# Optimization experiments

Hardware: AMD Instinct MI355X
Metric: run time of the kernel (lower is better)

## Reference

```python
import jax, jax.numpy as jnp
import numpy as np
from jax import lax

B, C, H, W = 8192, 256, 5, 5
G = 8
SE_HID = 64        # max(8, 256 // 4)
GN_EPS = 1e-5
MM_EPS = 1e-8


def group_norm(x, gamma, beta):
    # x: [B, C, H, W]; normalize per (group, H, W)
    b = x.shape[0]
    xg = x.reshape(b, G, C // G, H, W)
    mean = xg.mean(axis=(2, 3, 4), keepdims=True)
    var = xg.var(axis=(2, 3, 4), keepdims=True)
    xg = (xg - mean) * lax.rsqrt(var + GN_EPS)
    xn = xg.reshape(b, C, H, W)
    return xn * gamma[None, :, None, None] + beta[None, :, None, None]


def setup_inputs() -> dict:
    key = jax.random.key(0)
    ks = jax.random.split(key, 10)
    x = jax.random.normal(ks[0], (B, C, H, W), dtype=jnp.float32)
    pair_mask = (jax.random.uniform(ks[1], (B, 1, H, W)) < 0.8).astype(jnp.float32)
    s1 = 1.0 / np.sqrt(C)
    W1 = jax.random.normal(ks[2], (C, C), dtype=jnp.float32) * s1          # 1x1 conv
    W2 = jax.random.normal(ks[3], (C, C, 3, 3), dtype=jnp.float32) * (s1 / 3.0)
    g1 = jnp.ones((C,), jnp.float32); b1 = jnp.zeros((C,), jnp.float32)
    g2 = jnp.ones((C,), jnp.float32); b2 = jnp.zeros((C,), jnp.float32)
    fc1_w = jax.random.normal(ks[4], (SE_HID, C), dtype=jnp.float32) * s1
    fc1_b = jnp.zeros((SE_HID,), jnp.float32)
    fc2_w = jax.random.normal(ks[5], (C, SE_HID), dtype=jnp.float32) / np.sqrt(SE_HID)
    fc2_b = jnp.zeros((C,), jnp.float32)
    return {"x": x, "pair_mask": pair_mask, "W1": W1, "g1": g1, "b1": b1,
            "W2": W2, "g2": g2, "b2": b2,
            "fc1_w": fc1_w, "fc1_b": fc1_b, "fc2_w": fc2_w, "fc2_b": fc2_b}


def reference(x, pair_mask, W1, g1, b1, W2, g2, b2, fc1_w, fc1_b, fc2_w, fc2_b):
    residual = x
    # conv1: 1x1, no bias -> channel mixing
    out = jnp.einsum('bchw,oc->bohw', x, W1)
    out = jax.nn.gelu(group_norm(out, g1, b1), approximate=False)
    # conv2: 3x3, padding=1, no bias
    out = lax.conv_general_dilated(out, W2, window_strides=(1, 1),
                                   padding=((1, 1), (1, 1)),
                                   dimension_numbers=('NCHW', 'OIHW', 'NCHW'))
    out = jax.nn.gelu(group_norm(out, g2, b2), approximate=False)
    out = out + residual
    # masked SE
    denom = jnp.maximum(pair_mask.sum(axis=(-1, -2)), MM_EPS)   # [B,1]
    pooled = (out * pair_mask).sum(axis=(-1, -2)) / denom       # [B,C]
    h = jax.nn.gelu(pooled @ fc1_w.T + fc1_b, approximate=False)
    gate = jax.nn.sigmoid(h @ fc2_w.T + fc2_b)                  # [B,C]
    out = out * gate[:, :, None, None] * pair_mask              # SE mask
    out = out * pair_mask                                       # final mask
    return out, gate
```

## Files before the change

### kernel.cpp

```cpp
#include <hip/hip_runtime.h>
#include <math.h>


typedef short v8s  __attribute__((ext_vector_type(8)));
typedef short v4s  __attribute__((ext_vector_type(4)));
typedef float v16f __attribute__((ext_vector_type(16)));
typedef float v4f  __attribute__((ext_vector_type(4)));

#define NTHREADS 512
#define NB 2
#define CPB 560
#define YROWS 49
#define YSB (YROWS*CPB)

#define Y_BYTES  (NB*YSB)
#define GB_OFF   (Y_BYTES)
#define MASK_OFF (GB_OFF + 4096)
#define POOL_OFF (MASK_OFF + 256)
#define H_OFF    (POOL_OFF + 2048)
#define GATE_OFF (H_OFF + 512)
#define INVD_OFF (GATE_OFF + 2048)
#define SMEM_BYTES (INVD_OFF + 64)

__device__ __forceinline__ unsigned short f2bf(float f){
  unsigned u = __float_as_uint(f);
  u = u + 0x7fffu + ((u >> 16) & 1u);
  return (unsigned short)(u >> 16);
}
__device__ __forceinline__ float gelu_f(float v){
  float z  = fabsf(v) * 0.70710678118654752f;
  float t  = __builtin_amdgcn_rcpf(fmaf(0.3275911f, z, 1.0f));
  float e  = __builtin_amdgcn_exp2f(-z*z*1.4426950408889634f);
  float p  = fmaf(1.061405429f, t, -1.453152027f);
  p = fmaf(p, t, 1.421413741f);
  p = fmaf(p, t, -0.284496736f);
  p = fmaf(p, t, 0.254829592f);
  float er = fmaf(-p*t, e, 1.0f);
  er = __builtin_copysignf(er, v);
  return 0.5f*v*(1.0f + er);
}

__device__ __forceinline__ void v16store(char* dst, const v16f &v){
  #pragma unroll
  for (int q=0;q<4;++q){
    v4f t; t[0]=v[4*q]; t[1]=v[4*q+1]; t[2]=v[4*q+2]; t[3]=v[4*q+3];
    *(v4f*)(dst + q*1024) = t;
  }
}
__device__ __forceinline__ void v16addload(const char* src, v16f &v){
  #pragma unroll
  for (int q=0;q<4;++q){
    v4f t = *(const v4f*)(src + q*1024);
    v[4*q]+=t[0]; v[4*q+1]+=t[1]; v[4*q+2]+=t[2]; v[4*q+3]+=t[3];
  }
}

__global__ void prep_kernel(const float* __restrict__ W1, const float* __restrict__ W2,
                            const float* __restrict__ fc1w, const float* __restrict__ fc2w,
                            unsigned short* __restrict__ w1p, unsigned short* __restrict__ w2p,
                            float* __restrict__ fc1t, float* __restrict__ fc2t)
{
  int t = blockIdx.x*blockDim.x + threadIdx.x;
  int stride = gridDim.x*blockDim.x;
  for (int i=t; i<16*256*16; i+=stride){
    int s=i>>12, o=(i>>4)&255, kk=i&15;
    w1p[i] = f2bf(W1[o*256 + s*16 + kk]);
  }
  for (int i=t; i<144*256*16; i+=stride){
    int s=i>>12, o=(i>>4)&255, kk=i&15;
    int tap=s>>4, cb=s&15;
    w2p[i] = f2bf(W2[o*2304 + (cb*16+kk)*9 + tap]);
  }
  for (int i=t; i<256*64; i+=stride){ int c=i>>6, h=i&63; fc1t[i]=fc1w[h*256+c]; }
  for (int i=t; i<64*256; i+=stride){ int k=i>>8, c=i&255; fc2t[i]=fc2w[c*64+k]; }
}

__global__ __launch_bounds__(NTHREADS, 4) void lrb_main(
    const float* __restrict__ xg, const float* __restrict__ maskg,
    const float* __restrict__ g1, const float* __restrict__ b1,
    const float* __restrict__ g2, const float* __restrict__ b2,
    const unsigned short* __restrict__ w1p, const unsigned short* __restrict__ w2p,
    const float* __restrict__ fc1t, const float* __restrict__ fc1b,
    const float* __restrict__ fc2t, const float* __restrict__ fc2b,
    float* __restrict__ outg, float* __restrict__ gateg)
{
  extern __shared__ char smem[];
  float* OUTF = (float*)smem;
  float* GB   = (float*)(smem + GB_OFF);
  float* MS   = (float*)(smem + MASK_OFF);
  float* POOL = (float*)(smem + POOL_OFF);
  float* HS   = (float*)(smem + H_OFF);
  float* GT   = (float*)(smem + GATE_OFF);
  float* INVD = (float*)(smem + INVD_OFF);

  const int tid  = threadIdx.x;
  const int lane = tid & 63;
  const int wid  = tid >> 6;
  const int mp   = wid >> 1;
  const int kh   = wid & 1;
  const int p    = lane & 31;
  const int half = lane >> 5;
  const int hx   = half << 4;
  const bool pv  = (p < 25);
  const int b0   = blockIdx.x * NB;

  {
    int4 z4; z4.x=z4.y=z4.z=z4.w=0;
    for (int i = tid; i < NB*24*35; i += NTHREADS){
      int nbb = i / 840;
      int rem = i - nbb*840;
      int rr  = 25 + rem/35, cc = rem - (rem/35)*35;
      *(int4*)(smem + nbb*YSB + rr*CPB + cc*16) = z4;
    }
    if (tid < 256){
      GB[tid]=g1[tid]; GB[256+tid]=b1[tid]; GB[512+tid]=g2[tid]; GB[768+tid]=b2[tid];
    }
    if (tid >= 256 && tid < 256 + NB*32){
      int t2 = tid - 256;
      int nbb = t2>>5, pp = t2&31;
      MS[t2] = (pp < 25) ? maskg[(size_t)(b0+nbb)*25 + pp] : 0.f;
    }
  }

  const int pr = p/5, ps = p - 5*(p/5);
  const int pbase = pv ? (7*pr + ps) : 0;
  const int pbCPB = pbase*CPB;
  const int zCPB  = (p-24)*CPB;
  const int bcol  = hx + kh*256;
  const char* w1c = (const char*)w1p;
  const char* w2c = (const char*)w2p;
  const int aoff1 = (wid*32 + p)*32 + hx;
  const char* w2base = w2c + kh*65536 + mp*2048 + p*32 + hx;
  const char* Yb1[2] = { smem + p*CPB + hx, smem + YSB + p*CPB + hx };

  v8s A1[3], B1[3][2];
  #pragma unroll
  for (int s0=0; s0<3; ++s0) A1[s0] = *(const v8s*)(w1c + s0*8192 + aoff1);

  for (int i = tid; i < NB*25*32; i += NTHREADS){
    int nbb = i / 800;
    int rem = i - nbb*800;
    int pp  = rem >> 5;
    int c8  = rem & 31;
    const float* src = xg + ((size_t)(b0+nbb)*256 + c8*8)*25 + pp;
    v8s pk;
    #pragma unroll
    for (int k=0;k<8;++k) pk[k] = (short)f2bf(src[k*25]);
    *(v8s*)(smem + nbb*YSB + pp*CPB + c8*16) = pk;
  }
  __syncthreads();

  if (tid < NB){
    float s=0.f;
    #pragma unroll
    for (int pp=0;pp<25;++pp) s += MS[tid*32+pp];
    INVD[tid] = __builtin_amdgcn_rcpf(fmaxf(s, 1e-8f));
  }

  v16f acc1_0, acc1_1;
  #pragma unroll
  for (int j=0;j<16;++j){ acc1_0[j]=0.f; acc1_1[j]=0.f; }
  #pragma unroll
  for (int s0=0; s0<3; ++s0){
    B1[s0][0] = *(const v8s*)(Yb1[0] + s0*32);
    B1[s0][1] = *(const v8s*)(Yb1[1] + s0*32);
  }
  #pragma unroll
  for (int s=0; s<16; ++s){
    acc1_0 = __builtin_amdgcn_mfma_f32_32x32x16_bf16(A1[s%3], B1[s%3][0], acc1_0, 0,0,0);
    acc1_1 = __builtin_amdgcn_mfma_f32_32x32x16_bf16(A1[s%3], B1[s%3][1], acc1_1, 0,0,0);
    if (s+3 < 16){
      A1[s%3] = *(const v8s*)(w1c + (s+3)*8192 + aoff1);
      B1[s%3][0] = *(const v8s*)(Yb1[0] + (s+3)*32);
      B1[s%3][1] = *(const v8s*)(Yb1[1] + (s+3)*32);
    }
  }

  {
    float s0a=0.f,q0a=0.f,s1a=0.f,q1a=0.f;
    #pragma unroll
    for (int j=0;j<16;++j){
      float v0 = acc1_0[j], v1 = acc1_1[j];
      s0a+=v0; q0a+=v0*v0; s1a+=v1; q1a+=v1*v1;
    }
    #pragma unroll
    for (int off=1; off<64; off<<=1){
      s0a += __shfl_xor(s0a, off, 64); q0a += __shfl_xor(q0a, off, 64);
      s1a += __shfl_xor(s1a, off, 64); q1a += __shfl_xor(q1a, off, 64);
    }
    __syncthreads();

    const int grow = pbase + 8;
    float mu0 = s0a*(1.f/800.f), mu1 = s1a*(1.f/800.f);
    float rstd0 = rsqrtf(q0a*(1.f/800.f) - mu0*mu0 + 1e-5f);
    float rstd1 = rsqrtf(q1a*(1.f/800.f) - mu1*mu1 + 1e-5f);
    if (pv){
      #pragma unroll
      for (int nt=0; nt<2; ++nt){
        float mu = nt ? mu1 : mu0, rstd = nt ? rstd1 : rstd0;
        char* dst = smem + nt*YSB + grow*CPB + wid*64 + half*8;
        #pragma unroll
        for (int q=0;q<4;++q){
          v4s pk;
          #pragma unroll
          for (int i2=0;i2<4;++i2){
            int ch = wid*32 + q*8 + half*4 + i2;
            float v = nt ? acc1_1[4*q+i2] : acc1_0[4*q+i2];
            float f = (v-mu)*rstd*GB[ch]+GB[256+ch];
            pk[i2] = (short)f2bf(gelu_f(f));
          }
          *(v4s*)(dst + q*16) = pk;
        }
      }
    }
  }
  {
    int4 z4; z4.x=z4.y=z4.z=z4.w=0;
    for (int i = tid; i < NB*12*35; i += NTHREADS){
      int nbb = i / 420;
      int rem = i - nbb*420;
      int rr  = rem/35, cc = rem - (rem/35)*35;
      int row = rr < 8 ? rr : (rr < 10 ? rr + 5 : rr + 10);
      *(int4*)(smem + nbb*YSB + row*CPB + cc*16) = z4;
    }
  }

  v8s A2[3][2], B2[3][2];
  #pragma unroll
  for (int s0=0; s0<3; ++s0){
    A2[s0][0] = *(const v8s*)(w2base + (s0>>3)*131072 + (s0&7)*8192);
    A2[s0][1] = *(const v8s*)(w2base + (s0>>3)*131072 + (s0&7)*8192 + 1024);
  }
  __syncthreads();

  v16f acc2_00, acc2_01, acc2_10, acc2_11;
  #pragma unroll
  for (int j=0;j<16;++j){ acc2_00[j]=0.f; acc2_01[j]=0.f; acc2_10[j]=0.f; acc2_11[j]=0.f; }

  {
    constexpr int OFF7[9] = {0,1,2,7,8,9,14,15,16};
    #pragma unroll
    for (int s0=0; s0<3; ++s0){
      int ro = pv ? (pbCPB + OFF7[0]*CPB) : zCPB;
      B2[s0][0] = *(const v8s*)(smem + ro + bcol + (s0&7)*32);
      B2[s0][1] = *(const v8s*)(smem + YSB + ro + bcol + (s0&7)*32);
    }
    #pragma unroll
    for (int s=0; s<72; ++s){
      acc2_00 = __builtin_amdgcn_mfma_f32_32x32x16_bf16(A2[s%3][0], B2[s%3][0], acc2_00, 0,0,0);
      acc2_01 = __builtin_amdgcn_mfma_f32_32x32x16_bf16(A2[s%3][0], B2[s%3][1], acc2_01, 0,0,0);
      acc2_10 = __builtin_amdgcn_mfma_f32_32x32x16_bf16(A2[s%3][1], B2[s%3][0], acc2_10, 0,0,0);
      acc2_11 = __builtin_amdgcn_mfma_f32_32x32x16_bf16(A2[s%3][1], B2[s%3][1], acc2_11, 0,0,0);
      if (s+3 < 72){
        int s3 = s+3;
        A2[s%3][0] = *(const v8s*)(w2base + (s3>>3)*131072 + (s3&7)*8192);
        A2[s%3][1] = *(const v8s*)(w2base + (s3>>3)*131072 + (s3&7)*8192 + 1024);
        int ro = pv ? (pbCPB + OFF7[s3>>3]*CPB) : zCPB;
        B2[s%3][0] = *(const v8s*)(smem + ro + bcol + (s3&7)*32);
        B2[s%3][1] = *(const v8s*)(smem + YSB + ro + bcol + (s3&7)*32);
      }
    }
  }
  __syncthreads();

  {
    char* EXw = smem + (kh^1)*16384 + mp*4096 + (lane<<4);
    const char* EXr = smem + kh*16384 + mp*4096 + (lane<<4);
    if (kh==0) v16store(EXw, acc2_01); else v16store(EXw, acc2_00);
    __syncthreads();
    if (kh==0) v16addload(EXr, acc2_00); else v16addload(EXr, acc2_01);
    __syncthreads();
    if (kh==0) v16store(EXw, acc2_11); else v16store(EXw, acc2_10);
    __syncthreads();
    if (kh==0) v16addload(EXr, acc2_10); else v16addload(EXr, acc2_11);
  }
  v16f F0 = (kh==0) ? acc2_00 : acc2_01;
  v16f F1 = (kh==0) ? acc2_10 : acc2_11;

  {
    float s0a=0.f,q0a=0.f,s1a=0.f,q1a=0.f;
    #pragma unroll
    for (int j=0;j<16;++j){
      float v0=F0[j], v1=F1[j];
      s0a+=v0; q0a+=v0*v0; s1a+=v1; q1a+=v1*v1;
    }
    #pragma unroll
    for (int off=1; off<64; off<<=1){
      s0a += __shfl_xor(s0a, off, 64); q0a += __shfl_xor(q0a, off, 64);
      s1a += __shfl_xor(s1a, off, 64); q1a += __shfl_xor(q1a, off, 64);
    }
    __syncthreads();

    float mu0 = s0a*(1.f/800.f), mu1 = s1a*(1.f/800.f);
    float rstd0 = rsqrtf(q0a*(1.f/800.f) - mu0*mu0 + 1e-5f);
    float rstd1 = rsqrtf(q1a*(1.f/800.f) - mu1*mu1 + 1e-5f);
    float mk = pv ? MS[kh*32+p] : 0.f;
    const float* xr = xg + ((size_t)(b0+kh)*256 + mp*64)*25 + p;
    float ps0[16], ps1[16];
    #pragma unroll
    for (int j=0;j<16;++j){
      int crow = (j&3) + 8*(j>>2) + 4*half;
      {
        int ch = mp*64 + crow;
        float f = (F0[j]-mu0)*rstd0*GB[512+ch]+GB[768+ch];
        f = gelu_f(f);
        if (pv){ f += xr[crow*25]; OUTF[kh*6400 + ch*25 + p] = f; }
        ps0[j] = f*mk;
      }
      {
        int ch = mp*64 + 32 + crow;
        float f = (F1[j]-mu1)*rstd1*GB[512+ch]+GB[768+ch];
        f = gelu_f(f);
        if (pv){ f += xr[(32+crow)*25]; OUTF[kh*6400 + ch*25 + p] = f; }
        ps1[j] = f*mk;
      }
    }
    #pragma unroll
    for (int off=1; off<32; off<<=1)
      #pragma unroll
      for (int j=0;j<16;++j){
        ps0[j] += __shfl_xor(ps0[j], off, 64);
        ps1[j] += __shfl_xor(ps1[j], off, 64);
      }
    if ((lane&31)==0){
      #pragma unroll
      for (int j=0;j<16;++j){
        int crow = (j&3) + 8*(j>>2) + 4*half;
        POOL[kh*256 + mp*64 + crow]      = ps0[j];
        POOL[kh*256 + mp*64 + 32 + crow] = ps1[j];
      }
    }
  }
  __syncthreads();

  {
    int nbb  = tid >> 8;
    int hid  = (tid >> 2) & 63;
    int part = tid & 3;
    const float* pl = POOL + nbb*256 + part*64;
    const float* wp = fc1t + part*64*64 + hid;
    float dot = 0.f;
    #pragma unroll 8
    for (int c=0;c<64;++c) dot += wp[c*64]*pl[c];
    dot += __shfl_xor(dot, 1, 64);
    dot += __shfl_xor(dot, 2, 64);
    if (part == 0)
      HS[nbb*64+hid] = gelu_f(fmaf(INVD[nbb], dot, fc1b[hid]));
  }
  __syncthreads();
  {
    int ch = tid & 255, nbb = tid >> 8;
    const float* hp = HS + nbb*64;
    float dot = 0.f;
    #pragma unroll 8
    for (int k=0;k<64;++k) dot += fc2t[k*256+ch]*hp[k];
    dot += fc2b[ch];
    float gv = __builtin_amdgcn_rcpf(1.0f + __builtin_amdgcn_exp2f(-dot*1.4426950408889634f));
    GT[nbb*256+ch] = gv;
    gateg[(size_t)(b0+nbb)*256+ch] = gv;
  }
  __syncthreads();

  for (int i = tid; i < NB*1600; i += NTHREADS){
    int nbb = i / 1600;
    int r4  = i - nbb*1600;
    int e0  = r4*4;
    v4f o4 = *(const v4f*)(OUTF + nbb*6400 + e0);
    #pragma unroll
    for (int k=0;k<4;++k){
      int e = e0+k;
      int ch = e/25;
      int pp = e - ch*25;
      o4[k] = o4[k] * GT[nbb*256+ch] * MS[nbb*32+pp];
    }
    *(v4f*)(outg + (size_t)(b0+nbb)*6400 + e0) = o4;
  }
}

extern "C" void kernel_launch(void* const* d_in, const int* in_sizes, int n_in,
                              void* d_out, int out_size, void* d_ws, size_t ws_size,
                              hipStream_t stream)
{
  const float* xg   = (const float*)d_in[0];
  const float* pm   = (const float*)d_in[1];
  const float* W1   = (const float*)d_in[2];
  const float* g1   = (const float*)d_in[3];
  const float* b1   = (const float*)d_in[4];
  const float* W2   = (const float*)d_in[5];
  const float* g2   = (const float*)d_in[6];
  const float* b2   = (const float*)d_in[7];
  const float* fc1w = (const float*)d_in[8];
  const float* fc1b = (const float*)d_in[9];
  const float* fc2w = (const float*)d_in[10];
  const float* fc2b = (const float*)d_in[11];

  float* outg  = (float*)d_out;
  float* gateg = outg + (size_t)8192*256*25;

  unsigned short* w1p = (unsigned short*)d_ws;
  unsigned short* w2p = w1p + 16*256*16;
  float* fc1t = (float*)(w2p + 144*256*16);
  float* fc2t = fc1t + 256*64;

  prep_kernel<<<dim3(512), dim3(256), 0, stream>>>(W1, W2, fc1w, fc2w, w1p, w2p, fc1t, fc2t);

  hipFuncSetAttribute(reinterpret_cast<const void*>(lrb_main),
                      hipFuncAttributeMaxDynamicSharedMemorySize, (int)SMEM_BYTES);
  lrb_main<<<dim3(4096), dim3(NTHREADS), SMEM_BYTES, stream>>>(
      xg, pm, g1, b1, g2, b2, w1p, w2p, fc1t, fc1b, fc2t, fc2b, outg, gateg);
}
```

Measured before the change: 615.7 us.

## Restructure conv2 loop per row-tap, add MFMA priority, pool via LDS dot

Repacks W2 so each K-half's taps are laid out contiguously and rewrites the 72-step conv2 MFMA loop as three row passes of 24 steps. Each pass uses a base-offset increment instead of per-step OFF7 table lookups. Adds s_setprio around MFMA groups in both GEMMs so matrix instructions get issue priority over loads. Replaces the shuffle-based masked pooling (16x2 values over 5 xor rounds) with a per-thread 25-element dot over LDS after an extra barrier. The change trades shuffle work and address arithmetic for one more sync and a rolled outer loop.

```diff
diff --git a/kernel.cpp b/kernel.cpp
--- a/kernel.cpp
+++ b/kernel.cpp
@@ -68,8 +68,11 @@
   }
   for (int i=t; i<144*256*16; i+=stride){
     int s=i>>12, o=(i>>4)&255, kk=i&15;
-    int tap=s>>4, cb=s&15;
-    w2p[i] = f2bf(W2[o*2304 + (cb*16+kk)*9 + tap]);
+    int kh = (s >= 72) ? 1 : 0;
+    int r  = s - kh*72;
+    int tap = r>>3, u = r&7;
+    int ck = kh*128 + u*16 + kk;
+    w2p[i] = f2bf(W2[o*2304 + ck*9 + tap]);
   }
   for (int i=t; i<256*64; i+=stride){ int c=i>>6, h=i&63; fc1t[i]=fc1w[h*256+c]; }
   for (int i=t; i<64*256; i+=stride){ int k=i>>8, c=i&255; fc2t[i]=fc2w[c*64+k]; }
@@ -124,13 +127,11 @@
 
   const int pr = p/5, ps = p - 5*(p/5);
   const int pbase = pv ? (7*pr + ps) : 0;
-  const int pbCPB = pbase*CPB;
-  const int zCPB  = (p-24)*CPB;
   const int bcol  = hx + kh*256;
   const char* w1c = (const char*)w1p;
   const char* w2c = (const char*)w2p;
   const int aoff1 = (wid*32 + p)*32 + hx;
-  const char* w2base = w2c + kh*65536 + mp*2048 + p*32 + hx;
+  const char* w2k = w2c + kh*589824 + mp*2048 + p*32 + hx;
   const char* Yb1[2] = { smem + p*CPB + hx, smem + YSB + p*CPB + hx };
 
   v8s A1[3], B1[3][2];
@@ -167,8 +168,10 @@
   }
   #pragma unroll
   for (int s=0; s<16; ++s){
+    __builtin_amdgcn_s_setprio(1);
     acc1_0 = __builtin_amdgcn_mfma_f32_32x32x16_bf16(A1[s%3], B1[s%3][0], acc1_0, 0,0,0);
     acc1_1 = __builtin_amdgcn_mfma_f32_32x32x16_bf16(A1[s%3], B1[s%3][1], acc1_1, 0,0,0);
+    __builtin_amdgcn_s_setprio(0);
     if (s+3 < 16){
       A1[s%3] = *(const v8s*)(w1c + (s+3)*8192 + aoff1);
       B1[s%3][0] = *(const v8s*)(Yb1[0] + (s+3)*32);
@@ -228,8 +231,8 @@
   v8s A2[3][2], B2[3][2];
   #pragma unroll
   for (int s0=0; s0<3; ++s0){
-    A2[s0][0] = *(const v8s*)(w2base + (s0>>3)*131072 + (s0&7)*8192);
-    A2[s0][1] = *(const v8s*)(w2base + (s0>>3)*131072 + (s0&7)*8192 + 1024);
+    A2[s0][0] = *(const v8s*)(w2k + s0*8192);
+    A2[s0][1] = *(const v8s*)(w2k + s0*8192 + 1024);
   }
   __syncthreads();
 
@@ -238,28 +241,46 @@
   for (int j=0;j<16;++j){ acc2_00[j]=0.f; acc2_01[j]=0.f; acc2_10[j]=0.f; acc2_11[j]=0.f; }
 
   {
-    constexpr int OFF7[9] = {0,1,2,7,8,9,14,15,16};
+    int bq = pv ? pbase*CPB : 41*CPB;
+    const int bd = pv ? 7*CPB : 0;
+    int tb = 0;
+
     #pragma unroll
     for (int s0=0; s0<3; ++s0){
-      int ro = pv ? (pbCPB + OFF7[0]*CPB) : zCPB;
-      B2[s0][0] = *(const v8s*)(smem + ro + bcol + (s0&7)*32);
-      B2[s0][1] = *(const v8s*)(smem + YSB + ro + bcol + (s0&7)*32);
-    }
-    #pragma unroll
-    for (int s=0; s<72; ++s){
-      acc2_00 = __builtin_amdgcn_mfma_f32_32x32x16_bf16(A2[s%3][0], B2[s%3][0], acc2_00, 0,0,0);
-      acc2_01 = __builtin_amdgcn_mfma_f32_32x32x16_bf16(A2[s%3][0], B2[s%3][1], acc2_01, 0,0,0);
-      acc2_10 = __builtin_amdgcn_mfma_f32_32x32x16_bf16(A2[s%3][1], B2[s%3][0], acc2_10, 0,0,0);
-      acc2_11 = __builtin_amdgcn_mfma_f32_32x32x16_bf16(A2[s%3][1], B2[s%3][1], acc2_11, 0,0,0);
-      if (s+3 < 72){
-        int s3 = s+3;
-        A2[s%3][0] = *(const v8s*)(w2base + (s3>>3)*131072 + (s3&7)*8192);
-        A2[s%3][1] = *(const v8s*)(w2base + (s3>>3)*131072 + (s3&7)*8192 + 1024);
-        int ro = pv ? (pbCPB + OFF7[s3>>3]*CPB) : zCPB;
-        B2[s%3][0] = *(const v8s*)(smem + ro + bcol + (s3&7)*32);
-        B2[s%3][1] = *(const v8s*)(smem + YSB + ro + bcol + (s3&7)*32);
-      }
-    }
+      B2[s0][0] = *(const v8s*)(smem + bq + bcol + s0*32);
+      B2[s0][1] = *(const v8s*)(smem + YSB + bq + bcol + s0*32);
+    }
+
+#define C2_STEP(S, PF) do { \
+    __builtin_amdgcn_s_setprio(1); \
+    acc2_00 = __builtin_amdgcn_mfma_f32_32x32x16_bf16(A2[(S)%3][0], B2[(S)%3][0], acc2_00, 0,0,0); \
+    acc2_01 = __builtin_amdgcn_mfma_f32_32x32x16_bf16(A2[(S)%3][0], B2[(S)%3][1], acc2_01, 0,0,0); \
+    acc2_10 = __builtin_amdgcn_mfma_f32_32x32x16_bf16(A2[(S)%3][1], B2[(S)%3][0], acc2_10, 0,0,0); \
+    acc2_11 = __builtin_amdgcn_mfma_f32_32x32x16_bf16(A2[(S)%3][1], B2[(S)%3][1], acc2_11, 0,0,0); \
+    __builtin_amdgcn_s_setprio(0); \
+    if (PF) { \
+      const char* ap_ = w2k + tb + ((S)+3)*8192; \
+      A2[(S)%3][0] = *(const v8s*)(ap_); \
+      A2[(S)%3][1] = *(const v8s*)(ap_ + 1024); \
+      const int ro_ = (((S)+3) < 24) ? (((S)+3)>>3)*CPB : 7*CPB; \
+      const int co_ = (((S)+3)&7)*32; \
+      B2[(S)%3][0] = *(const v8s*)(smem + bq + ro_ + bcol + co_); \
+      B2[(S)%3][1] = *(const v8s*)(smem + YSB + bq + ro_ + bcol + co_); \
+    } \
+  } while(0)
+
+    #pragma unroll 1
+    for (int tr=0; tr<2; ++tr){
+      #pragma unroll
+      for (int s=0; s<24; ++s) C2_STEP(s, 1);
+      tb += 196608;
+      bq += bd;
+    }
+    #pragma unroll
+    for (int s=0; s<21; ++s) C2_STEP(s, 1);
+    #pragma unroll
+    for (int s=21; s<24; ++s) C2_STEP(s, 0);
+#undef C2_STEP
   }
   __syncthreads();
 
@@ -294,42 +315,36 @@
     float mu0 = s0a*(1.f/800.f), mu1 = s1a*(1.f/800.f);
     float rstd0 = rsqrtf(q0a*(1.f/800.f) - mu0*mu0 + 1e-5f);
     float rstd1 = rsqrtf(q1a*(1.f/800.f) - mu1*mu1 + 1e-5f);
-    float mk = pv ? MS[kh*32+p] : 0.f;
     const float* xr = xg + ((size_t)(b0+kh)*256 + mp*64)*25 + p;
-    float ps0[16], ps1[16];
-    #pragma unroll
-    for (int j=0;j<16;++j){
-      int crow = (j&3) + 8*(j>>2) + 4*half;
-      {
-        int ch = mp*64 + crow;
-        float f = (F0[j]-mu0)*rstd0*GB[512+ch]+GB[768+ch];
-        f = gelu_f(f);
-        if (pv){ f += xr[crow*25]; OUTF[kh*6400 + ch*25 + p] = f; }
-        ps0[j] = f*mk;
-      }
-      {
-        int ch = mp*64 + 32 + crow;
-        float f = (F1[j]-mu1)*rstd1*GB[512+ch]+GB[768+ch];
-        f = gelu_f(f);
-        if (pv){ f += xr[(32+crow)*25]; OUTF[kh*6400 + ch*25 + p] = f; }
-        ps1[j] = f*mk;
-      }
-    }
-    #pragma unroll
-    for (int off=1; off<32; off<<=1)
-      #pragma unroll
-      for (int j=0;j<16;++j){
-        ps0[j] += __shfl_xor(ps0[j], off, 64);
-        ps1[j] += __shfl_xor(ps1[j], off, 64);
-      }
-    if ((lane&31)==0){
+    if (pv){
       #pragma unroll
       for (int j=0;j<16;++j){
         int crow = (j&3) + 8*(j>>2) + 4*half;
-        POOL[kh*256 + mp*64 + crow]      = ps0[j];
-        POOL[kh*256 + mp*64 + 32 + crow] = ps1[j];
+        {
+          int ch = mp*64 + crow;
+          float f = (F0[j]-mu0)*rstd0*GB[512+ch]+GB[768+ch];
+          f = gelu_f(f) + xr[crow*25];
+          OUTF[kh*6400 + ch*25 + p] = f;
+        }
+        {
+          int ch = mp*64 + 32 + crow;
+          float f = (F1[j]-mu1)*rstd1*GB[512+ch]+GB[768+ch];
+          f = gelu_f(f) + xr[(32+crow)*25];
+          OUTF[kh*6400 + ch*25 + p] = f;
+        }
       }
     }
+  }
+  __syncthreads();
+
+  {
+    int nbb = tid >> 8, ch = tid & 255;
+    const float* of = OUTF + nbb*6400 + ch*25;
+    const float* ms = MS + nbb*32;
+    float dot = 0.f;
+    #pragma unroll
+    for (int pp=0; pp<25; ++pp) dot = fmaf(of[pp], ms[pp], dot);
+    POOL[nbb*256 + ch] = dot;
   }
   __syncthreads();
 
```

Measured after the change: 540.6 us. -12.2%, faster.
